# Kernel tuning notes

Hardware: AMD Instinct MI355X
Metric: run time of the kernel (lower is better)

The kernel has to match this reference:

```python
import jax, jax.numpy as jnp
import numpy as np

B, S, U, M = 4096, 64, 128, 32
ODE_UNFOLDS = 6
EPS = 1e-08

def _uniform(k, shape, lo, hi):
    return jax.random.uniform(k, shape, jnp.float32, lo, hi)

def setup_inputs() -> dict:
    key = jax.random.key(0)
    ks = jax.random.split(key, 16)
    return {
        "inputs": jax.random.normal(ks[0], (B, S), jnp.float32),
        "state": jax.random.normal(ks[1], (B, U), jnp.float32),
        "gleak": _uniform(ks[2], (U,), 0.001, 1.0),
        "vleak": _uniform(ks[3], (U,), -0.2, 0.2),
        "cm": _uniform(ks[4], (U,), 0.4, 0.6),
        "sigma": _uniform(ks[5], (U, U), 3.0, 8.0),
        "mu": _uniform(ks[6], (U, U), 0.3, 0.8),
        "w": _uniform(ks[7], (U, U), 0.001, 1.0),
        "erev": jnp.sign(jax.random.normal(ks[8], (U, U), jnp.float32)),
        "sensory_sigma": _uniform(ks[9], (S, U), 3.0, 8.0),
        "sensory_mu": _uniform(ks[10], (S, U), 0.3, 0.8),
        "sensory_w": _uniform(ks[11], (S, U), 0.001, 1.0),
        "sensory_erev": jnp.sign(jax.random.normal(ks[12], (S, U), jnp.float32)),
        "sparsity_mask": (jax.random.uniform(ks[13], (U, U)) < 0.5).astype(jnp.float32),
        "sensory_sparsity_mask": (jax.random.uniform(ks[14], (S, U)) < 0.5).astype(jnp.float32),
        "input_w": jnp.ones((S,), jnp.float32),
        "input_b": jnp.zeros((S,), jnp.float32),
        "output_w": jnp.ones((M,), jnp.float32),
        "output_b": jnp.zeros((M,), jnp.float32),
    }

def reference(inputs, state, gleak, vleak, cm, sigma, mu, w, erev,
              sensory_sigma, sensory_mu, sensory_w, sensory_erev,
              sparsity_mask, sensory_sparsity_mask,
              input_w, input_b, output_w, output_b):
    # input mapping (affine)
    x = inputs * input_w + input_b                       # [B,S]
    # sensory synapse activation: [B,S,U]
    sens_act = (sensory_w * sensory_sparsity_mask) * jax.nn.sigmoid(
        sensory_sigma * (x[:, :, None] - sensory_mu))
    w_num_sensory = jnp.sum(sens_act * sensory_erev, axis=1)   # [B,U]
    w_den_sensory = jnp.sum(sens_act, axis=1)                  # [B,U]

    wm = w * sparsity_mask                                     # masked weights [U,U]
    wme = wm * erev                                            # weights*erev   [U,U]
    cm_t = cm * ODE_UNFOLDS                                    # cm / (1/unfolds)
    leak = gleak * vleak

    v = state
    for _ in range(ODE_UNFOLDS):
        sig = jax.nn.sigmoid(sigma * (v[:, :, None] - mu))     # [B,U,U] (src,dst)
        w_num = jnp.einsum('bsu,su->bu', sig, wme) + w_num_sensory
        w_den = jnp.einsum('bsu,su->bu', sig, wm) + w_den_sensory
        v = (cm_t * v + leak + w_num) / (cm_t + gleak + w_den + EPS)

    out = v[:, :M] * output_w + output_b                       # motor slice + affine
    return out, v
```

## Files before the change

### kernel.cpp

```cpp
#include <hip/hip_runtime.h>
#include <hip/hip_fp16.h>

typedef unsigned short u16;
typedef unsigned int   u32;

#define B_TOTAL 4096
#define NU      128
#define NS      64
#define NM      32
#define UNFOLDS 6
#define LOG2E   1.44269504088896340736f

__device__ __forceinline__ float bf2f(u16 v) {
  return __uint_as_float(((u32)v) << 16);
}
__device__ __forceinline__ u16 f2bf(float f) {
  u32 x = __float_as_uint(f);
  return (u16)((x + 0x7fffu + ((x >> 16) & 1u)) >> 16);
}

template<bool BF16>
__device__ __forceinline__ float LD(const void* p, int i) {
  if (BF16) return bf2f(((const u16*)p)[i]);
  return ((const float*)p)[i];
}

__device__ __forceinline__ float rdlane(float v, int lane) {
  return __int_as_float(__builtin_amdgcn_readlane(__float_as_int(v), lane));
}

__device__ __forceinline__ u32 pk(float a, float b) {
  __half2 h = __halves2half2(__float2half_rn(a), __float2half_rn(b));
  return __builtin_bit_cast(u32, h);
}
__device__ __forceinline__ float lo2f(u32 h) {
  return __low2float(__builtin_bit_cast(__half2, h));
}
__device__ __forceinline__ float hi2f(u32 h) {
  return __high2float(__builtin_bit_cast(__half2, h));
}

__device__ __forceinline__ void step2i(uint4 a, float va, float vb,
                                       float& na0, float& da0, float& na1, float& da1,
                                       float& nb0, float& db0, float& nb1, float& db1) {
  float ta0 = fmaf(va, lo2f(a.x), lo2f(a.y));
  float ta1 = fmaf(va, hi2f(a.x), hi2f(a.y));
  float tb0 = fmaf(vb, lo2f(a.x), lo2f(a.y));
  float tb1 = fmaf(vb, hi2f(a.x), hi2f(a.y));
  float ea0 = __builtin_amdgcn_exp2f(ta0);
  float ea1 = __builtin_amdgcn_exp2f(ta1);
  float eb0 = __builtin_amdgcn_exp2f(tb0);
  float eb1 = __builtin_amdgcn_exp2f(tb1);
  float pa0 = 1.0f + ea0, pa1 = 1.0f + ea1;
  float pb0 = 1.0f + eb0, pb1 = 1.0f + eb1;
  float ra = __builtin_amdgcn_rcpf(pa0 * pa1);
  float rb = __builtin_amdgcn_rcpf(pb0 * pb1);
  float sa0 = pa1 * ra, sa1 = pa0 * ra;
  float sb0 = pb1 * rb, sb1 = pb0 * rb;
  na0 = fmaf(sa0, lo2f(a.z), na0);  da0 = fmaf(sa0, lo2f(a.w), da0);
  na1 = fmaf(sa1, hi2f(a.z), na1);  da1 = fmaf(sa1, hi2f(a.w), da1);
  nb0 = fmaf(sb0, lo2f(a.z), nb0);  db0 = fmaf(sb0, lo2f(a.w), db0);
  nb1 = fmaf(sb1, hi2f(a.z), nb1);  db1 = fmaf(sb1, hi2f(a.w), db1);
}

template<bool BF16>
__device__ __forceinline__ void body(
    const void* g_in, const void* g_state, const void* g_gleak, const void* g_vleak,
    const void* g_cm, const void* g_sigma, const void* g_mu, const void* g_w,
    const void* g_erev, const void* g_ssig, const void* g_smu, const void* g_sw,
    const void* g_serev, const void* g_mask, const void* g_smask,
    const void* g_iw, const void* g_ib, const void* g_ow, const void* g_ob,
    void* g_out,
    uint4* smR)
{
  const int tid = threadIdx.x;
  const int b0  = blockIdx.x * 16;

  const int r  = tid >> 6;
  const int u0 = tid & 63;
  const int u1 = u0 + 64;
  const int ba = b0 + 2 * r;
  const int bb = ba + 1;

  #pragma unroll 2
  for (int e = tid; e < NS * 64; e += 512) {
    int s = e >> 6, l = e & 63;
    int i0 = s * NU + l, i1 = i0 + 64;
    float sl0 = LD<BF16>(g_ssig, i0) * LOG2E, sl1 = LD<BF16>(g_ssig, i1) * LOG2E;
    float ms0 = LD<BF16>(g_smu, i0) * sl0,    ms1 = LD<BF16>(g_smu, i1) * sl1;
    float w0 = LD<BF16>(g_sw, i0) * LD<BF16>(g_smask, i0) * LD<BF16>(g_serev, i0);
    float w1 = LD<BF16>(g_sw, i1) * LD<BF16>(g_smask, i1) * LD<BF16>(g_serev, i1);
    smR[e] = make_uint4(pk(-sl0, -sl1), pk(ms0, ms1), pk(w0, w1),
                        pk(fabsf(w0), fabsf(w1)));
  }
  __syncthreads();

  float iw = LD<BF16>(g_iw, u0), ib = LD<BF16>(g_ib, u0);
  float xa = LD<BF16>(g_in, ba * NS + u0) * iw + ib;
  float xb = LD<BF16>(g_in, bb * NS + u0) * iw + ib;
  float va0 = LD<BF16>(g_state, ba * NU + u0);
  float va1 = LD<BF16>(g_state, ba * NU + u1);
  float vb0 = LD<BF16>(g_state, bb * NU + u0);
  float vb1 = LD<BF16>(g_state, bb * NU + u1);
  const float gl0 = LD<BF16>(g_gleak, u0), gl1 = LD<BF16>(g_gleak, u1);
  const float lk0 = gl0 * LD<BF16>(g_vleak, u0);
  const float lk1 = gl1 * LD<BF16>(g_vleak, u1);
  const float cm0 = LD<BF16>(g_cm, u0) * (float)UNFOLDS;
  const float cm1 = LD<BF16>(g_cm, u1) * (float)UNFOLDS;

  const uint4* pR = smR + u0;

  float nsa0 = 0.f, dsa0 = 0.f, nsa1 = 0.f, dsa1 = 0.f;
  float nsb0 = 0.f, dsb0 = 0.f, nsb1 = 0.f, dsb1 = 0.f;
  #pragma unroll 8
  for (int s = 0; s < NS; ++s) {
    float xsa = rdlane(xa, s);
    float xsb = rdlane(xb, s);
    uint4 a = pR[s * 64];
    step2i(a, xsa, xsb, nsa0, dsa0, nsa1, dsa1, nsb0, dsb0, nsb1, dsb1);
  }
  __syncthreads();

  #pragma unroll 4
  for (int e = tid; e < NU * 64; e += 512) {
    int j = e >> 6, l = e & 63;
    int i0 = j * NU + l, i1 = i0 + 64;
    float sl0 = LD<BF16>(g_sigma, i0) * LOG2E, sl1 = LD<BF16>(g_sigma, i1) * LOG2E;
    float ms0 = LD<BF16>(g_mu, i0) * sl0,      ms1 = LD<BF16>(g_mu, i1) * sl1;
    float w0 = LD<BF16>(g_w, i0) * LD<BF16>(g_mask, i0) * LD<BF16>(g_erev, i0);
    float w1 = LD<BF16>(g_w, i1) * LD<BF16>(g_mask, i1) * LD<BF16>(g_erev, i1);
    smR[e] = make_uint4(pk(-sl0, -sl1), pk(ms0, ms1), pk(w0, w1),
                        pk(fabsf(w0), fabsf(w1)));
  }
  __syncthreads();

  #pragma unroll 1
  for (int it = 0; it < UNFOLDS; ++it) {
    float na0 = nsa0, da0 = dsa0, na1 = nsa1, da1 = dsa1;
    float nb0 = nsb0, db0 = dsb0, nb1 = nsb1, db1 = dsb1;
    #pragma unroll 8
    for (int j = 0; j < 64; ++j) {
      float vja = rdlane(va0, j);
      float vjb = rdlane(vb0, j);
      uint4 a = pR[j * 64];
      step2i(a, vja, vjb, na0, da0, na1, da1, nb0, db0, nb1, db1);
    }
    #pragma unroll 8
    for (int j = 0; j < 64; ++j) {
      float vja = rdlane(va1, j);
      float vjb = rdlane(vb1, j);
      uint4 a = pR[(j + 64) * 64];
      step2i(a, vja, vjb, na0, da0, na1, da1, nb0, db0, nb1, db1);
    }
    va0 = fmaf(cm0, va0, lk0 + na0) * __builtin_amdgcn_rcpf(cm0 + gl0 + da0 + 1e-8f);
    va1 = fmaf(cm1, va1, lk1 + na1) * __builtin_amdgcn_rcpf(cm1 + gl1 + da1 + 1e-8f);
    vb0 = fmaf(cm0, vb0, lk0 + nb0) * __builtin_amdgcn_rcpf(cm0 + gl0 + db0 + 1e-8f);
    vb1 = fmaf(cm1, vb1, lk1 + nb1) * __builtin_amdgcn_rcpf(cm1 + gl1 + db1 + 1e-8f);
  }

  if (BF16) {
    u16* om = (u16*)g_out;
    u16* ov = om + B_TOTAL * NM;
    ov[ba * NU + u0] = f2bf(va0);
    ov[ba * NU + u1] = f2bf(va1);
    ov[bb * NU + u0] = f2bf(vb0);
    ov[bb * NU + u1] = f2bf(vb1);
    if (u0 < NM) {
      float ow = LD<true>(g_ow, u0), ob = LD<true>(g_ob, u0);
      om[ba * NM + u0] = f2bf(fmaf(va0, ow, ob));
      om[bb * NM + u0] = f2bf(fmaf(vb0, ow, ob));
    }
  } else {
    float* om = (float*)g_out;
    float* ov = om + B_TOTAL * NM;
    ov[ba * NU + u0] = va0;
    ov[ba * NU + u1] = va1;
    ov[bb * NU + u0] = vb0;
    ov[bb * NU + u1] = vb1;
    if (u0 < NM) {
      float ow = LD<false>(g_ow, u0), ob = LD<false>(g_ob, u0);
      om[ba * NM + u0] = fmaf(va0, ow, ob);
      om[bb * NM + u0] = fmaf(vb0, ow, ob);
    }
  }
}

__global__ __launch_bounds__(512, 2) void ltc_kernel(
    const void* g_in, const void* g_state, const void* g_gleak, const void* g_vleak,
    const void* g_cm, const void* g_sigma, const void* g_mu, const void* g_w,
    const void* g_erev, const void* g_ssig, const void* g_smu, const void* g_sw,
    const void* g_serev, const void* g_mask, const void* g_smask,
    const void* g_iw, const void* g_ib, const void* g_ow, const void* g_ob,
    void* g_out)
{
  __shared__ uint4 smR[NU * 64];

  const u16* sg = (const u16*)g_sigma;
  int cnt = 0;
  #pragma unroll
  for (int i = 0; i < 32; ++i) {
    float f = bf2f(sg[2 * i]);
    cnt += (f >= 2.0f && f <= 16.0f) ? 1 : 0;
  }
  if (cnt >= 24)
    body<true >(g_in, g_state, g_gleak, g_vleak, g_cm, g_sigma, g_mu, g_w, g_erev,
                g_ssig, g_smu, g_sw, g_serev, g_mask, g_smask,
                g_iw, g_ib, g_ow, g_ob, g_out, smR);
  else
    body<false>(g_in, g_state, g_gleak, g_vleak, g_cm, g_sigma, g_mu, g_w, g_erev,
                g_ssig, g_smu, g_sw, g_serev, g_mask, g_smask,
                g_iw, g_ib, g_ow, g_ob, g_out, smR);
}

extern "C" void kernel_launch(void* const* d_in, const int* in_sizes, int n_in,
                              void* d_out, int out_size, void* d_ws, size_t ws_size,
                              hipStream_t stream) {
  (void)in_sizes; (void)n_in; (void)out_size; (void)d_ws; (void)ws_size;
  dim3 grid(B_TOTAL / 16);
  dim3 block(512);
  hipLaunchKernelGGL(ltc_kernel, grid, block, 0, stream,
                     d_in[0], d_in[1], d_in[2], d_in[3], d_in[4],
                     d_in[5], d_in[6], d_in[7], d_in[8],
                     d_in[9], d_in[10], d_in[11], d_in[12],
                     d_in[13], d_in[14], d_in[15], d_in[16],
                     d_in[17], d_in[18], d_out);
}
```

Measured before the change: 209.7 us.

## Use one batch row per wavefront with 1024-thread blocks

Each wavefront now handles a single batch row instead of two, and blocks grow to 1024 threads so a block still covers 16 rows. This halves the register work per thread and doubles the number of waves, aiming for more latency hiding and occupancy. The cost is that each shared-memory parameter load now feeds one sigmoid pair instead of two, so LDS traffic per unit of arithmetic doubles. The launch bounds are raised to 1024 threads with 4 blocks requested, which constrains register allocation.

```diff
diff --git a/kernel.cpp b/kernel.cpp
--- a/kernel.cpp
+++ b/kernel.cpp
@@ -40,27 +40,17 @@
   return __high2float(__builtin_bit_cast(__half2, h));
 }
 
-__device__ __forceinline__ void step2i(uint4 a, float va, float vb,
-                                       float& na0, float& da0, float& na1, float& da1,
-                                       float& nb0, float& db0, float& nb1, float& db1) {
-  float ta0 = fmaf(va, lo2f(a.x), lo2f(a.y));
-  float ta1 = fmaf(va, hi2f(a.x), hi2f(a.y));
-  float tb0 = fmaf(vb, lo2f(a.x), lo2f(a.y));
-  float tb1 = fmaf(vb, hi2f(a.x), hi2f(a.y));
-  float ea0 = __builtin_amdgcn_exp2f(ta0);
-  float ea1 = __builtin_amdgcn_exp2f(ta1);
-  float eb0 = __builtin_amdgcn_exp2f(tb0);
-  float eb1 = __builtin_amdgcn_exp2f(tb1);
-  float pa0 = 1.0f + ea0, pa1 = 1.0f + ea1;
-  float pb0 = 1.0f + eb0, pb1 = 1.0f + eb1;
-  float ra = __builtin_amdgcn_rcpf(pa0 * pa1);
-  float rb = __builtin_amdgcn_rcpf(pb0 * pb1);
-  float sa0 = pa1 * ra, sa1 = pa0 * ra;
-  float sb0 = pb1 * rb, sb1 = pb0 * rb;
-  na0 = fmaf(sa0, lo2f(a.z), na0);  da0 = fmaf(sa0, lo2f(a.w), da0);
-  na1 = fmaf(sa1, hi2f(a.z), na1);  da1 = fmaf(sa1, hi2f(a.w), da1);
-  nb0 = fmaf(sb0, lo2f(a.z), nb0);  db0 = fmaf(sb0, lo2f(a.w), db0);
-  nb1 = fmaf(sb1, hi2f(a.z), nb1);  db1 = fmaf(sb1, hi2f(a.w), db1);
+__device__ __forceinline__ void step1i(uint4 a, float v,
+                                       float& n0, float& d0, float& n1, float& d1) {
+  float t0 = fmaf(v, lo2f(a.x), lo2f(a.y));
+  float t1 = fmaf(v, hi2f(a.x), hi2f(a.y));
+  float e0 = __builtin_amdgcn_exp2f(t0);
+  float e1 = __builtin_amdgcn_exp2f(t1);
+  float p0 = 1.0f + e0, p1 = 1.0f + e1;
+  float rr = __builtin_amdgcn_rcpf(p0 * p1);
+  float s0 = p1 * rr, s1 = p0 * rr;
+  n0 = fmaf(s0, lo2f(a.z), n0);  d0 = fmaf(s0, lo2f(a.w), d0);
+  n1 = fmaf(s1, hi2f(a.z), n1);  d1 = fmaf(s1, hi2f(a.w), d1);
 }
 
 template<bool BF16>
@@ -76,14 +66,13 @@
   const int tid = threadIdx.x;
   const int b0  = blockIdx.x * 16;
 
-  const int r  = tid >> 6;
-  const int u0 = tid & 63;
-  const int u1 = u0 + 64;
-  const int ba = b0 + 2 * r;
-  const int bb = ba + 1;
+  const int r   = tid >> 6;
+  const int u0  = tid & 63;
+  const int u1  = u0 + 64;
+  const int row = b0 + r;
 
-  #pragma unroll 2
-  for (int e = tid; e < NS * 64; e += 512) {
+  #pragma unroll 4
+  for (int e = tid; e < NS * 64; e += 1024) {
     int s = e >> 6, l = e & 63;
     int i0 = s * NU + l, i1 = i0 + 64;
     float sl0 = LD<BF16>(g_ssig, i0) * LOG2E, sl1 = LD<BF16>(g_ssig, i1) * LOG2E;
@@ -96,12 +85,9 @@
   __syncthreads();
 
   float iw = LD<BF16>(g_iw, u0), ib = LD<BF16>(g_ib, u0);
-  float xa = LD<BF16>(g_in, ba * NS + u0) * iw + ib;
-  float xb = LD<BF16>(g_in, bb * NS + u0) * iw + ib;
-  float va0 = LD<BF16>(g_state, ba * NU + u0);
-  float va1 = LD<BF16>(g_state, ba * NU + u1);
-  float vb0 = LD<BF16>(g_state, bb * NU + u0);
-  float vb1 = LD<BF16>(g_state, bb * NU + u1);
+  float x  = LD<BF16>(g_in, row * NS + u0) * iw + ib;
+  float v0 = LD<BF16>(g_state, row * NU + u0);
+  float v1 = LD<BF16>(g_state, row * NU + u1);
   const float gl0 = LD<BF16>(g_gleak, u0), gl1 = LD<BF16>(g_gleak, u1);
   const float lk0 = gl0 * LD<BF16>(g_vleak, u0);
   const float lk1 = gl1 * LD<BF16>(g_vleak, u1);
@@ -110,19 +96,16 @@
 
   const uint4* pR = smR + u0;
 
-  float nsa0 = 0.f, dsa0 = 0.f, nsa1 = 0.f, dsa1 = 0.f;
-  float nsb0 = 0.f, dsb0 = 0.f, nsb1 = 0.f, dsb1 = 0.f;
+  float ns0 = 0.f, ds0 = 0.f, ns1 = 0.f, ds1 = 0.f;
   #pragma unroll 8
   for (int s = 0; s < NS; ++s) {
-    float xsa = rdlane(xa, s);
-    float xsb = rdlane(xb, s);
-    uint4 a = pR[s * 64];
-    step2i(a, xsa, xsb, nsa0, dsa0, nsa1, dsa1, nsb0, dsb0, nsb1, dsb1);
+    float xs = rdlane(x, s);
+    step1i(pR[s * 64], xs, ns0, ds0, ns1, ds1);
   }
   __syncthreads();
 
-  #pragma unroll 4
-  for (int e = tid; e < NU * 64; e += 512) {
+  #pragma unroll 8
+  for (int e = tid; e < NU * 64; e += 1024) {
     int j = e >> 6, l = e & 63;
     int i0 = j * NU + l, i1 = i0 + 64;
     float sl0 = LD<BF16>(g_sigma, i0) * LOG2E, sl1 = LD<BF16>(g_sigma, i1) * LOG2E;
@@ -136,56 +119,43 @@
 
   #pragma unroll 1
   for (int it = 0; it < UNFOLDS; ++it) {
-    float na0 = nsa0, da0 = dsa0, na1 = nsa1, da1 = dsa1;
-    float nb0 = nsb0, db0 = dsb0, nb1 = nsb1, db1 = dsb1;
+    float n0 = ns0, d0 = ds0, n1 = ns1, d1 = ds1;
     #pragma unroll 8
     for (int j = 0; j < 64; ++j) {
-      float vja = rdlane(va0, j);
-      float vjb = rdlane(vb0, j);
-      uint4 a = pR[j * 64];
-      step2i(a, vja, vjb, na0, da0, na1, da1, nb0, db0, nb1, db1);
+      float vj = rdlane(v0, j);
+      step1i(pR[j * 64], vj, n0, d0, n1, d1);
     }
     #pragma unroll 8
     for (int j = 0; j < 64; ++j) {
-      float vja = rdlane(va1, j);
-      float vjb = rdlane(vb1, j);
-      uint4 a = pR[(j + 64) * 64];
-      step2i(a, vja, vjb, na0, da0, na1, da1, nb0, db0, nb1, db1);
+      float vj = rdlane(v1, j);
+      step1i(pR[(j + 64) * 64], vj, n0, d0, n1, d1);
     }
-    va0 = fmaf(cm0, va0, lk0 + na0) * __builtin_amdgcn_rcpf(cm0 + gl0 + da0 + 1e-8f);
-    va1 = fmaf(cm1, va1, lk1 + na1) * __builtin_amdgcn_rcpf(cm1 + gl1 + da1 + 1e-8f);
-    vb0 = fmaf(cm0, vb0, lk0 + nb0) * __builtin_amdgcn_rcpf(cm0 + gl0 + db0 + 1e-8f);
-    vb1 = fmaf(cm1, vb1, lk1 + nb1) * __builtin_amdgcn_rcpf(cm1 + gl1 + db1 + 1e-8f);
+    v0 = fmaf(cm0, v0, lk0 + n0) * __builtin_amdgcn_rcpf(cm0 + gl0 + d0 + 1e-8f);
+    v1 = fmaf(cm1, v1, lk1 + n1) * __builtin_amdgcn_rcpf(cm1 + gl1 + d1 + 1e-8f);
   }
 
   if (BF16) {
     u16* om = (u16*)g_out;
     u16* ov = om + B_TOTAL * NM;
-    ov[ba * NU + u0] = f2bf(va0);
-    ov[ba * NU + u1] = f2bf(va1);
-    ov[bb * NU + u0] = f2bf(vb0);
-    ov[bb * NU + u1] = f2bf(vb1);
+    ov[row * NU + u0] = f2bf(v0);
+    ov[row * NU + u1] = f2bf(v1);
     if (u0 < NM) {
       float ow = LD<true>(g_ow, u0), ob = LD<true>(g_ob, u0);
-      om[ba * NM + u0] = f2bf(fmaf(va0, ow, ob));
-      om[bb * NM + u0] = f2bf(fmaf(vb0, ow, ob));
+      om[row * NM + u0] = f2bf(fmaf(v0, ow, ob));
     }
   } else {
     float* om = (float*)g_out;
     float* ov = om + B_TOTAL * NM;
-    ov[ba * NU + u0] = va0;
-    ov[ba * NU + u1] = va1;
-    ov[bb * NU + u0] = vb0;
-    ov[bb * NU + u1] = vb1;
+    ov[row * NU + u0] = v0;
+    ov[row * NU + u1] = v1;
     if (u0 < NM) {
       float ow = LD<false>(g_ow, u0), ob = LD<false>(g_ob, u0);
-      om[ba * NM + u0] = fmaf(va0, ow, ob);
-      om[bb * NM + u0] = fmaf(vb0, ow, ob);
+      om[row * NM + u0] = fmaf(v0, ow, ob);
     }
   }
 }
 
-__global__ __launch_bounds__(512, 2) void ltc_kernel(
+__global__ __launch_bounds__(1024, 4) void ltc_kernel(
     const void* g_in, const void* g_state, const void* g_gleak, const void* g_vleak,
     const void* g_cm, const void* g_sigma, const void* g_mu, const void* g_w,
     const void* g_erev, const void* g_ssig, const void* g_smu, const void* g_sw,
@@ -217,7 +187,7 @@
                               hipStream_t stream) {
   (void)in_sizes; (void)n_in; (void)out_size; (void)d_ws; (void)ws_size;
   dim3 grid(B_TOTAL / 16);
-  dim3 block(512);
+  dim3 block(1024);
   hipLaunchKernelGGL(ltc_kernel, grid, block, 0, stream,
                      d_in[0], d_in[1], d_in[2], d_in[3], d_in[4],
                      d_in[5], d_in[6], d_in[7], d_in[8],
```

New measurement: 215.2 us. +2.7%, slower.
